# Kernel tuning notes

Hardware: AMD Instinct MI355X
Metric: run time of the kernel (lower is better)

The kernel has to match this reference:

```python
import jax, jax.numpy as jnp
import numpy as np
import math

B, S, D = 4, 2048, 1024

def setup_inputs() -> dict:
    key = jax.random.key(0)
    ks = jax.random.split(key, 8)
    scale = 1.0 / math.sqrt(D)
    x = jax.random.normal(ks[0], (B, S, D), dtype=jnp.float32)
    # additive causal mask: 0 on/below diag, -1e9 above (broadcast over batch)
    causal = jnp.where(jnp.tril(jnp.ones((S, S), dtype=bool)), 0.0, -1e9).astype(jnp.float32)
    mask = jnp.broadcast_to(causal, (B, S, S))
    Wq = jax.random.uniform(ks[1], (D, D), jnp.float32, -scale, scale)
    bq = jax.random.uniform(ks[2], (D,), jnp.float32, -scale, scale)
    Wk = jax.random.uniform(ks[3], (D, D), jnp.float32, -scale, scale)
    bk = jax.random.uniform(ks[4], (D,), jnp.float32, -scale, scale)
    Wv = jax.random.uniform(ks[5], (D, D), jnp.float32, -scale, scale)
    bv = jax.random.uniform(ks[6], (D,), jnp.float32, -scale, scale)
    return {"x": x, "mask": mask, "Wq": Wq, "bq": bq, "Wk": Wk, "bk": bk, "Wv": Wv, "bv": bv}

def reference(x, mask, Wq, bq, Wk, bk, Wv, bv):
    q = jnp.einsum('bsd,de->bse', x, Wq) + bq
    k = jnp.einsum('bsd,de->bse', x, Wk) + bk
    v = jnp.einsum('bsd,de->bse', x, Wv) + bv
    scores = jnp.einsum('bqd,bkd->bqk', q, k) / math.sqrt(k.shape[-1])
    attn = jax.nn.softmax(scores + mask, axis=-1)
    return jnp.einsum('bqk,bkd->bqd', attn, v)
```

## Files before the change

kernel.cpp:

```cpp
#include <hip/hip_runtime.h>
#include <hip/hip_bf16.h>
#include <hip/hip_fp16.h>
#include <math.h>

typedef short v8s __attribute__((ext_vector_type(8)));
typedef short v4s __attribute__((ext_vector_type(4)));
typedef float v4f __attribute__((ext_vector_type(4)));
typedef unsigned short ushort_t;

__device__ __forceinline__ unsigned short f2bf(float f) {
    unsigned int u = __float_as_uint(f);
    u = (u + 0x7FFFu + ((u >> 16) & 1u)) >> 16;
    return (unsigned short)u;
}
__device__ __forceinline__ unsigned short f2h(float f) {
    __half h = __float2half(f);
    return *reinterpret_cast<unsigned short*>(&h);
}
__device__ __forceinline__ float h2f(unsigned short u) {
    __half h = *reinterpret_cast<__half*>(&u);
    return __half2float(h);
}

__device__ __forceinline__ void load_lds16(const void* g, void* l) {
    __builtin_amdgcn_global_load_lds((const __attribute__((address_space(1))) void*)g,
                                     (__attribute__((address_space(3))) void*)l,
                                     16, 0, 0);
}

#define FENCE() asm volatile("" ::: "memory")
#define BAR() do { FENCE(); __builtin_amdgcn_s_barrier(); FENCE(); } while (0)
#define LGKM0() asm volatile("s_waitcnt lgkmcnt(0)" ::: "memory")
#define VMC(n) asm volatile("s_waitcnt vmcnt(" #n ")" ::: "memory")

__global__ __launch_bounds__(256)
void prep_kernel(const float4* __restrict__ x4, ushort_t* __restrict__ xb,
                 const float* __restrict__ W0, const float* __restrict__ W1,
                 const float* __restrict__ W2, ushort_t* __restrict__ Wt) {
    if (blockIdx.x < 2048) {
        int i = blockIdx.x * 256 + threadIdx.x;
        #pragma unroll
        for (int it = 0; it < 4; ++it, i += 524288) {
            float4 v = x4[i];
            v4s p;
            p[0] = (short)f2bf(v.x); p[1] = (short)f2bf(v.y);
            p[2] = (short)f2bf(v.z); p[3] = (short)f2bf(v.w);
            *(v4s*)(xb + (size_t)i * 4) = p;
        }
    } else {
        int f = blockIdx.x - 2048;
        int z = f >> 10; int rem = f & 1023;
        int n0 = (rem & 31) * 32, k0 = (rem >> 5) * 32;
        const float* W = (z == 0) ? W0 : (z == 1 ? W1 : W2);
        ushort_t* out = Wt + (size_t)z * 1024 * 1024;
        __shared__ float tile[32][33];
        int tx = threadIdx.x & 31, ty = threadIdx.x >> 5;
        #pragma unroll
        for (int i2 = 0; i2 < 32; i2 += 8)
            tile[ty + i2][tx] = W[(size_t)(k0 + ty + i2) * 1024 + n0 + tx];
        __syncthreads();
        #pragma unroll
        for (int i2 = 0; i2 < 32; i2 += 8)
            out[(size_t)(n0 + ty + i2) * 1024 + k0 + tx] = f2bf(tile[tx][ty + i2]);
    }
}

__global__ __launch_bounds__(512)
void gemm8_qkv(const ushort_t* __restrict__ A, const ushort_t* __restrict__ Bt,
               const float* __restrict__ bq, const float* __restrict__ bk,
               const float* __restrict__ bv,
               ushort_t* __restrict__ Qb, ushort_t* __restrict__ Kb,
               ushort_t* __restrict__ Vt)
{
    int f = blockIdx.x;
    int xcd = f & 7, i = f >> 3;
    const int by = xcd * 4 + (i >> 4);
    const int bx = i & 15;

    const int tid = threadIdx.x;
    const int lane = tid & 63, wid = tid >> 6;
    const int wm = wid >> 2, wc = wid & 3;
    const int frow = lane & 15, fq4 = lane >> 4;
    const bool bstager = (wid < 6);

    const int brow = by * 256, bcol = bx * 192;

    __shared__ ushort_t LA[2][2][256 * 32];
    __shared__ ushort_t LB[2][2][192 * 32];

    v4f acc[8][3];
    #pragma unroll
    for (int mi = 0; mi < 8; ++mi)
        #pragma unroll
        for (int ni = 0; ni < 3; ++ni)
            acc[mi][ni] = (v4f)0.f;

    const int srr = tid >> 2, sch = tid & 3;
    auto STA = [&](ushort_t* dst, int t, int kh) {
        #pragma unroll
        for (int c = 0; c < 2; ++c) {
            int r = c * 128 + srr;
            int ch = sch ^ ((r >> 1) & 3);
            load_lds16(A + (size_t)(brow + r) * 1024 + t * 64 + kh * 32 + ch * 8,
                       dst + (size_t)(c * 128 + srr) * 32 + sch * 8);
        }
    };
    auto STB = [&](ushort_t* dst, int t, int kh) {
        if (bstager) {
            #pragma unroll
            for (int c = 0; c < 2; ++c) {
                int ck = c * 384 + tid;
                int r = ck >> 2, s = ck & 3;
                int ch = s ^ ((r >> 1) & 3);
                load_lds16(Bt + (size_t)(bcol + r) * 1024 + t * 64 + kh * 32 + ch * 8,
                           dst + (size_t)ck * 8);
            }
        }
    };

    v8s a[4], b[3];
    const int rsw = fq4 ^ ((frow >> 1) & 3);
    auto RDA = [&](int buf, int kh, int mh) {
        #pragma unroll
        for (int i2 = 0; i2 < 4; ++i2) {
            int r = wm * 128 + (mh * 4 + i2) * 16 + frow;
            a[i2] = *(const v8s*)(&LA[buf][kh][(size_t)r * 32 + rsw * 8]);
        }
    };
    auto RDB = [&](int buf, int kh) {
        #pragma unroll
        for (int i2 = 0; i2 < 3; ++i2) {
            int r = wc * 48 + i2 * 16 + frow;
            b[i2] = *(const v8s*)(&LB[buf][kh][(size_t)r * 32 + rsw * 8]);
        }
    };
    auto MM = [&](int mh) {
        __builtin_amdgcn_s_setprio(1);
        #pragma unroll
        for (int i2 = 0; i2 < 4; ++i2)
            #pragma unroll
            for (int n = 0; n < 3; ++n)
                acc[mh * 4 + i2][n] =
                    __builtin_amdgcn_mfma_f32_16x16x32_bf16(a[i2], b[n], acc[mh * 4 + i2][n], 0, 0, 0);
        __builtin_amdgcn_s_setprio(0);
    };
    auto WAIT2 = [&]() { if (bstager) { VMC(4); } else { VMC(2); } };

    STA(LA[0][0], 0, 0); STB(LB[0][0], 0, 0);
    STA(LA[0][1], 0, 1); STB(LB[0][1], 0, 1);
    STA(LA[1][0], 1, 0); STB(LB[1][0], 1, 0);
    WAIT2(); BAR();

    for (int u = 0; u < 8; ++u) {
        const int t0 = 2 * u, t1 = 2 * u + 1;
        const bool pf = (u < 7);
        RDA(0, 0, 0); RDB(0, 0); STA(LA[1][1], t1, 1);
        BAR(); LGKM0(); MM(0); BAR();
        RDA(0, 0, 1); STB(LB[1][1], t1, 1);
        BAR(); LGKM0(); MM(1); BAR();
        RDA(0, 1, 0); RDB(0, 1); if (pf) STA(LA[0][0], t0 + 2, 0);
        BAR(); LGKM0(); MM(0); BAR();
        RDA(0, 1, 1);
        if (pf) { STB(LB[0][0], t0 + 2, 0); WAIT2(); }
        else    { VMC(0); }
        BAR(); LGKM0(); MM(1); BAR();
        RDA(1, 0, 0); RDB(1, 0); if (pf) STA(LA[0][1], t0 + 2, 1);
        BAR(); LGKM0(); MM(0); BAR();
        RDA(1, 0, 1); if (pf) STB(LB[0][1], t0 + 2, 1);
        BAR(); LGKM0(); MM(1); BAR();
        RDA(1, 1, 0); RDB(1, 1); if (pf) STA(LA[1][0], t1 + 2, 0);
        BAR(); LGKM0(); MM(0); BAR();
        RDA(1, 1, 1); if (pf) { STB(LB[1][0], t1 + 2, 0); WAIT2(); }
        BAR(); LGKM0(); MM(1); BAR();
    }

    const int fr = lane & 15;
    const int fq = lane >> 4;
    #pragma unroll
    for (int ni = 0; ni < 3; ++ni) {
        int gc = bx * 192 + wc * 48 + ni * 16 + fr;
        int route = gc >> 10;
        int cg = gc & 1023;
        if (route < 2) {
            ushort_t* C = route ? Kb : Qb;
            float bb = (route ? bk : bq)[cg];
            float scale = route ? 1.0f : 0.03125f;
            #pragma unroll
            for (int mi = 0; mi < 8; ++mi) {
                int gr0 = brow + wm * 128 + mi * 16 + fq * 4;
                #pragma unroll
                for (int j = 0; j < 4; ++j)
                    C[(size_t)(gr0 + j) * 1024 + cg] = f2bf((acc[mi][ni][j] + bb) * scale);
            }
        } else {
            float bb = bv[cg];
            #pragma unroll
            for (int mi = 0; mi < 8; ++mi) {
                int gr0 = brow + wm * 128 + mi * 16 + fq * 4;
                int bbat = gr0 >> 11;
                int sl2 = gr0 & 2047;
                alignas(8) ushort_t tmp[4];
                #pragma unroll
                for (int j = 0; j < 4; ++j)
                    tmp[j] = f2bf(acc[mi][ni][j] + bb);
                *(v4s*)(Vt + (size_t)bbat * (1024 * 2048) + (size_t)cg * 2048 + sl2) =
                    *(const v4s*)tmp;
            }
        }
    }
}

template <int MODE>
__global__ __launch_bounds__(256)
void gemm_ring(const ushort_t* __restrict__ A, int lda, long long strideA,
               const ushort_t* __restrict__ Bt, int ldb, long long strideB,
               void* __restrict__ Cv, int ldc, long long strideC, int K)
{
    int bx, by, bz;
    int f = blockIdx.x;
    if constexpr (MODE == 2) {
        int swz = (f & 7) * 68 + (f >> 3);
        bz = swz / 136; int t = swz % 136;
        int r = (int)((sqrtf(8.f * (float)t + 1.f) - 1.f) * 0.5f);
        while ((r + 1) * (r + 2) / 2 <= t) ++r;
        while (r * (r + 1) / 2 > t) --r;
        by = r; bx = t - r * (r + 1) / 2;
    } else {
        int swz = (f & 7) * 64 + (f >> 3);
        bz = swz >> 7; int rem = swz & 127;
        by = 15 - (rem >> 3); bx = rem & 7;
    }

    const int tid = threadIdx.x;
    const int lane = tid & 63, wid = tid >> 6;
    const int wm = wid >> 1, wc = wid & 1;

    const ushort_t* Ab = A + (size_t)bz * strideA;
    const ushort_t* Bb = Bt + (size_t)bz * strideB;

    __shared__ ushort_t As[3][128 * 32];
    __shared__ ushort_t Bs[3][128 * 32];

    const int brow = by * 128, bcol = bx * 128;

    int kEnd = K;
    if constexpr (MODE == 3) { int lim = (by + 1) * 128; kEnd = lim < K ? lim : K; }
    const int nt = kEnd / 32;

    v4f acc[4][4];
    #pragma unroll
    for (int mi = 0; mi < 4; ++mi)
        #pragma unroll
        for (int ni = 0; ni < 4; ++ni)
            acc[mi][ni] = (v4f)0.f;

    const int rr = tid >> 2, slot = tid & 3;
    auto STAGE = [&](int buf, int t) {
        const int k0 = t * 32;
        #pragma unroll
        for (int c = 0; c < 2; ++c) {
            int r = c * 64 + rr;
            int sc = ((slot ^ ((r >> 1) & 3)) << 3);
            load_lds16(Ab + (size_t)(brow + r) * lda + k0 + sc,
                       &As[buf][(size_t)(c * 64 + wid * 16) * 32]);
        }
        #pragma unroll
        for (int c = 0; c < 2; ++c) {
            int r = c * 64 + rr;
            int sc = ((slot ^ ((r >> 1) & 3)) << 3);
            load_lds16(Bb + (size_t)(bcol + r) * ldb + k0 + sc,
                       &Bs[buf][(size_t)(c * 64 + wid * 16) * 32]);
        }
    };

    const int frow = lane & 15, fq4 = lane >> 4;
    const int csw = ((fq4 ^ ((frow >> 1) & 3)) << 3);

    STAGE(0, 0);
    if (nt > 1) STAGE(1, 1);

    int cur = 0;
    for (int t = 0; t < nt; ++t) {
        if (t + 1 < nt) VMC(4); else VMC(0);
        BAR();
        if (t + 2 < nt) {
            int tgt = cur ? cur - 1 : 2;
            STAGE(tgt, t + 2);
        }
        const ushort_t* Ac = &As[cur][0];
        const ushort_t* Bc = &Bs[cur][0];
        v8s a[4], b[4];
        #pragma unroll
        for (int mi = 0; mi < 4; ++mi)
            a[mi] = *(const v8s*)(Ac + (size_t)(wm * 64 + mi * 16 + frow) * 32 + csw);
        #pragma unroll
        for (int ni = 0; ni < 4; ++ni)
            b[ni] = *(const v8s*)(Bc + (size_t)(wc * 64 + ni * 16 + frow) * 32 + csw);
        __builtin_amdgcn_s_setprio(1);
        #pragma unroll
        for (int mi = 0; mi < 4; ++mi)
            #pragma unroll
            for (int ni = 0; ni < 4; ++ni)
                acc[mi][ni] = __builtin_amdgcn_mfma_f32_16x16x32_bf16(a[mi], b[ni], acc[mi][ni], 0, 0, 0);
        __builtin_amdgcn_s_setprio(0);
        cur = (cur == 2) ? 0 : cur + 1;
    }

    const int fr = lane & 15;
    const int fq = lane >> 4;
    if constexpr (MODE == 2) {
        ushort_t* C = (ushort_t*)Cv + (size_t)bz * strideC;
        #pragma unroll
        for (int ni = 0; ni < 4; ++ni) {
            int gc = bcol + wc * 64 + ni * 16 + fr;
            #pragma unroll
            for (int mi = 0; mi < 4; ++mi) {
                int gr0 = brow + wm * 64 + mi * 16 + fq * 4;
                #pragma unroll
                for (int j = 0; j < 4; ++j)
                    C[(size_t)(gr0 + j) * ldc + gc] = f2h(acc[mi][ni][j]);
            }
        }
    } else {
        float* C = (float*)Cv + (size_t)bz * strideC;
        #pragma unroll
        for (int ni = 0; ni < 4; ++ni) {
            int gc = bcol + wc * 64 + ni * 16 + fr;
            #pragma unroll
            for (int mi = 0; mi < 4; ++mi) {
                int gr0 = brow + wm * 64 + mi * 16 + fq * 4;
                #pragma unroll
                for (int j = 0; j < 4; ++j)
                    C[(size_t)(gr0 + j) * ldc + gc] = acc[mi][ni][j];
            }
        }
    }
}

__global__ __launch_bounds__(256) void softmax_causal(ushort_t* __restrict__ Sc) {
    const int wid = threadIdx.x >> 6, lane = threadIdx.x & 63;
    const int row = blockIdx.x * 4 + wid;
    const int b = row >> 11, i = row & 2047;
    ushort_t* srow = Sc + ((size_t)b * 2048 + i) * 2048;
    const int L = i + 1;
    const int Lw = ((i >> 7) + 1) << 7;
    const int C4 = Lw >> 2;

    float v[8][4];
    const int NS = (C4 + 63) >> 6;

    float mx = -3.0e38f;
    #pragma unroll 8
    for (int s = 0; s < NS; ++s) {
        int c = lane + s * 64;
        if (c < C4) {
            v4s u = *(const v4s*)(srow + c * 4);
            #pragma unroll
            for (int e = 0; e < 4; ++e) {
                int j = c * 4 + e;
                float t = (j < L) ? h2f((unsigned short)u[e]) : -3.0e38f;
                v[s][e] = t;
                mx = fmaxf(mx, t);
            }
        }
    }
    #pragma unroll
    for (int o = 32; o; o >>= 1) mx = fmaxf(mx, __shfl_xor(mx, o));

    float sum = 0.f;
    #pragma unroll 8
    for (int s = 0; s < NS; ++s) {
        int c = lane + s * 64;
        if (c < C4) {
            #pragma unroll
            for (int e = 0; e < 4; ++e) {
                int j = c * 4 + e;
                float ev = (j < L) ? __expf(v[s][e] - mx) : 0.f;
                v[s][e] = ev;
                sum += ev;
            }
        }
    }
    #pragma unroll
    for (int o = 32; o; o >>= 1) sum += __shfl_xor(sum, o);
    const float inv = 1.f / sum;

    #pragma unroll 8
    for (int s = 0; s < NS; ++s) {
        int c = lane + s * 64;
        if (c < C4) {
            v4s p;
            #pragma unroll
            for (int e = 0; e < 4; ++e)
                p[e] = (short)f2bf(v[s][e] * inv);
            *(v4s*)(srow + c * 4) = p;
        }
    }
}

extern "C" void kernel_launch(void* const* d_in, const int* in_sizes, int n_in,
                              void* d_out, int out_size, void* d_ws, size_t ws_size,
                              hipStream_t stream) {
    const float* x  = (const float*)d_in[0];
    const float* Wq = (const float*)d_in[2];
    const float* bq = (const float*)d_in[3];
    const float* Wk = (const float*)d_in[4];
    const float* bk = (const float*)d_in[5];
    const float* Wv = (const float*)d_in[6];
    const float* bv = (const float*)d_in[7];

    ushort_t* xb = (ushort_t*)d_ws;
    ushort_t* Wt = xb + (size_t)8192 * 1024;
    ushort_t* Qb = Wt + (size_t)3 * 1024 * 1024;
    ushort_t* Kb = Qb + (size_t)8192 * 1024;
    ushort_t* Vt = Kb + (size_t)8192 * 1024;
    ushort_t* Sc = Vt + (size_t)8192 * 1024;

    prep_kernel<<<5120, 256, 0, stream>>>((const float4*)x, xb, Wq, Wk, Wv, Wt);

    gemm8_qkv<<<512, 512, 0, stream>>>(xb, Wt, bq, bk, bv, Qb, Kb, Vt);

    gemm_ring<2><<<544, 256, 0, stream>>>(Qb, 1024, 2048LL * 1024,
                                          Kb, 1024, 2048LL * 1024,
                                          Sc, 2048, 2048LL * 2048, 1024);

    softmax_causal<<<2048, 256, 0, stream>>>(Sc);

    gemm_ring<3><<<512, 256, 0, stream>>>(Sc, 2048, 2048LL * 2048,
                                          Vt, 2048, 2048LL * 1024,
                                          d_out, 1024, 2048LL * 1024, 2048);
    (void)in_sizes; (void)n_in; (void)out_size; (void)ws_size;
}
```

Baseline: 160.9 us.

## Switch QKV GEMM to 32x32x16 MFMA with 128x384 block tiles

The fused QKV projection GEMM now issues 32x32x16 bf16 MFMAs instead of 16x16x32, and the block tile changes from 256x192 to 128x384. LDS staging, fragment reads, the swizzle and the epilogue indexing are reworked to fit the new layout, and all 8 waves now stage B. Larger MFMAs cut the instruction count and the LDS fragment reads per flop. The new tile shape changes reuse and how many blocks the grid has, which may affect load balance.

```diff
diff --git a/kernel.cpp b/kernel.cpp
--- a/kernel.cpp
+++ b/kernel.cpp
@@ -6,6 +6,7 @@
 typedef short v8s __attribute__((ext_vector_type(8)));
 typedef short v4s __attribute__((ext_vector_type(4)));
 typedef float v4f __attribute__((ext_vector_type(4)));
+typedef float v16f __attribute__((ext_vector_type(16)));
 typedef unsigned short ushort_t;
 
 __device__ __forceinline__ unsigned short f2bf(float f) {
@@ -74,82 +75,81 @@
 {
     int f = blockIdx.x;
     int xcd = f & 7, i = f >> 3;
-    const int by = xcd * 4 + (i >> 4);
-    const int bx = i & 15;
+    const int by = xcd * 8 + (i >> 3);
+    const int bx = i & 7;
 
     const int tid = threadIdx.x;
     const int lane = tid & 63, wid = tid >> 6;
     const int wm = wid >> 2, wc = wid & 3;
-    const int frow = lane & 15, fq4 = lane >> 4;
-    const bool bstager = (wid < 6);
-
-    const int brow = by * 256, bcol = bx * 192;
-
-    __shared__ ushort_t LA[2][2][256 * 32];
-    __shared__ ushort_t LB[2][2][192 * 32];
-
-    v4f acc[8][3];
+    const int l31 = lane & 31, l5 = lane >> 5;
+
+    const int brow = by * 128, bcol = bx * 384;
+
+    __shared__ ushort_t LA[2][2][128 * 32];
+    __shared__ ushort_t LB[2][2][384 * 32];
+
+    v16f acc[2][3];
     #pragma unroll
-    for (int mi = 0; mi < 8; ++mi)
+    for (int mh = 0; mh < 2; ++mh)
         #pragma unroll
         for (int ni = 0; ni < 3; ++ni)
-            acc[mi][ni] = (v4f)0.f;
+            acc[mh][ni] = (v16f)0.f;
 
     const int srr = tid >> 2, sch = tid & 3;
     auto STA = [&](ushort_t* dst, int t, int kh) {
-        #pragma unroll
-        for (int c = 0; c < 2; ++c) {
-            int r = c * 128 + srr;
-            int ch = sch ^ ((r >> 1) & 3);
-            load_lds16(A + (size_t)(brow + r) * 1024 + t * 64 + kh * 32 + ch * 8,
-                       dst + (size_t)(c * 128 + srr) * 32 + sch * 8);
-        }
+        int r = srr;
+        int ch = sch ^ ((r >> 1) & 3);
+        load_lds16(A + (size_t)(brow + r) * 1024 + t * 64 + kh * 32 + ch * 8,
+                   dst + (size_t)r * 32 + sch * 8);
     };
     auto STB = [&](ushort_t* dst, int t, int kh) {
-        if (bstager) {
-            #pragma unroll
-            for (int c = 0; c < 2; ++c) {
-                int ck = c * 384 + tid;
-                int r = ck >> 2, s = ck & 3;
-                int ch = s ^ ((r >> 1) & 3);
-                load_lds16(Bt + (size_t)(bcol + r) * 1024 + t * 64 + kh * 32 + ch * 8,
-                           dst + (size_t)ck * 8);
-            }
-        }
-    };
-
-    v8s a[4], b[3];
-    const int rsw = fq4 ^ ((frow >> 1) & 3);
+        #pragma unroll
+        for (int c = 0; c < 3; ++c) {
+            int ck = c * 512 + tid;
+            int r = ck >> 2, s = ck & 3;
+            int ch = s ^ ((r >> 1) & 3);
+            load_lds16(Bt + (size_t)(bcol + r) * 1024 + t * 64 + kh * 32 + ch * 8,
+                       dst + (size_t)ck * 8);
+        }
+    };
+
+    v8s a[2], b[3][2];
     auto RDA = [&](int buf, int kh, int mh) {
-        #pragma unroll
-        for (int i2 = 0; i2 < 4; ++i2) {
-            int r = wm * 128 + (mh * 4 + i2) * 16 + frow;
-            a[i2] = *(const v8s*)(&LA[buf][kh][(size_t)r * 32 + rsw * 8]);
+        int r = wm * 64 + mh * 32 + l31;
+        int sw = (r >> 1) & 3;
+        #pragma unroll
+        for (int ks = 0; ks < 2; ++ks) {
+            int c = (ks * 2 + l5) ^ sw;
+            a[ks] = *(const v8s*)(&LA[buf][kh][(size_t)r * 32 + c * 8]);
         }
     };
     auto RDB = [&](int buf, int kh) {
         #pragma unroll
-        for (int i2 = 0; i2 < 3; ++i2) {
-            int r = wc * 48 + i2 * 16 + frow;
-            b[i2] = *(const v8s*)(&LB[buf][kh][(size_t)r * 32 + rsw * 8]);
+        for (int ni = 0; ni < 3; ++ni) {
+            int r = wc * 96 + ni * 32 + l31;
+            int sw = (r >> 1) & 3;
+            #pragma unroll
+            for (int ks = 0; ks < 2; ++ks) {
+                int c = (ks * 2 + l5) ^ sw;
+                b[ni][ks] = *(const v8s*)(&LB[buf][kh][(size_t)r * 32 + c * 8]);
+            }
         }
     };
     auto MM = [&](int mh) {
         __builtin_amdgcn_s_setprio(1);
         #pragma unroll
-        for (int i2 = 0; i2 < 4; ++i2)
-            #pragma unroll
-            for (int n = 0; n < 3; ++n)
-                acc[mh * 4 + i2][n] =
-                    __builtin_amdgcn_mfma_f32_16x16x32_bf16(a[i2], b[n], acc[mh * 4 + i2][n], 0, 0, 0);
+        for (int ni = 0; ni < 3; ++ni)
+            #pragma unroll
+            for (int ks = 0; ks < 2; ++ks)
+                acc[mh][ni] = __builtin_amdgcn_mfma_f32_32x32x16_bf16(
+                    a[ks], b[ni][ks], acc[mh][ni], 0, 0, 0);
         __builtin_amdgcn_s_setprio(0);
     };
-    auto WAIT2 = [&]() { if (bstager) { VMC(4); } else { VMC(2); } };
 
     STA(LA[0][0], 0, 0); STB(LB[0][0], 0, 0);
     STA(LA[0][1], 0, 1); STB(LB[0][1], 0, 1);
     STA(LA[1][0], 1, 0); STB(LB[1][0], 1, 0);
-    WAIT2(); BAR();
+    VMC(4); BAR();
 
     for (int u = 0; u < 8; ++u) {
         const int t0 = 2 * u, t1 = 2 * u + 1;
@@ -161,7 +161,7 @@
         RDA(0, 1, 0); RDB(0, 1); if (pf) STA(LA[0][0], t0 + 2, 0);
         BAR(); LGKM0(); MM(0); BAR();
         RDA(0, 1, 1);
-        if (pf) { STB(LB[0][0], t0 + 2, 0); WAIT2(); }
+        if (pf) { STB(LB[0][0], t0 + 2, 0); VMC(4); }
         else    { VMC(0); }
         BAR(); LGKM0(); MM(1); BAR();
         RDA(1, 0, 0); RDB(1, 0); if (pf) STA(LA[0][1], t0 + 2, 1);
@@ -170,41 +170,44 @@
         BAR(); LGKM0(); MM(1); BAR();
         RDA(1, 1, 0); RDB(1, 1); if (pf) STA(LA[1][0], t1 + 2, 0);
         BAR(); LGKM0(); MM(0); BAR();
-        RDA(1, 1, 1); if (pf) { STB(LB[1][0], t1 + 2, 0); WAIT2(); }
+        RDA(1, 1, 1); if (pf) { STB(LB[1][0], t1 + 2, 0); VMC(4); }
         BAR(); LGKM0(); MM(1); BAR();
     }
 
-    const int fr = lane & 15;
-    const int fq = lane >> 4;
     #pragma unroll
-    for (int ni = 0; ni < 3; ++ni) {
-        int gc = bx * 192 + wc * 48 + ni * 16 + fr;
-        int route = gc >> 10;
-        int cg = gc & 1023;
-        if (route < 2) {
-            ushort_t* C = route ? Kb : Qb;
-            float bb = (route ? bk : bq)[cg];
-            float scale = route ? 1.0f : 0.03125f;
-            #pragma unroll
-            for (int mi = 0; mi < 8; ++mi) {
-                int gr0 = brow + wm * 128 + mi * 16 + fq * 4;
+    for (int mh = 0; mh < 2; ++mh) {
+        #pragma unroll
+        for (int ni = 0; ni < 3; ++ni) {
+            int gc = bcol + wc * 96 + ni * 32 + l31;
+            int route = gc >> 10;
+            int cg = gc & 1023;
+            int grb = brow + wm * 64 + mh * 32 + 4 * l5;
+            if (route < 2) {
+                ushort_t* C = route ? Kb : Qb;
+                float bb = (route ? bk : bq)[cg];
+                float scale = route ? 1.0f : 0.03125f;
                 #pragma unroll
-                for (int j = 0; j < 4; ++j)
-                    C[(size_t)(gr0 + j) * 1024 + cg] = f2bf((acc[mi][ni][j] + bb) * scale);
-            }
-        } else {
-            float bb = bv[cg];
-            #pragma unroll
-            for (int mi = 0; mi < 8; ++mi) {
-                int gr0 = brow + wm * 128 + mi * 16 + fq * 4;
-                int bbat = gr0 >> 11;
-                int sl2 = gr0 & 2047;
-                alignas(8) ushort_t tmp[4];
+                for (int q = 0; q < 4; ++q) {
+                    #pragma unroll
+                    for (int jj = 0; jj < 4; ++jj) {
+                        int gr = grb + 8 * q + jj;
+                        C[(size_t)gr * 1024 + cg] =
+                            f2bf((acc[mh][ni][q * 4 + jj] + bb) * scale);
+                    }
+                }
+            } else {
+                float bb = bv[cg];
+                int bbat = grb >> 11;
                 #pragma unroll
-                for (int j = 0; j < 4; ++j)
-                    tmp[j] = f2bf(acc[mi][ni][j] + bb);
-                *(v4s*)(Vt + (size_t)bbat * (1024 * 2048) + (size_t)cg * 2048 + sl2) =
-                    *(const v4s*)tmp;
+                for (int q = 0; q < 4; ++q) {
+                    int s0 = (grb + 8 * q) & 2047;
+                    alignas(8) ushort_t tmp[4];
+                    #pragma unroll
+                    for (int jj = 0; jj < 4; ++jj)
+                        tmp[jj] = f2bf(acc[mh][ni][q * 4 + jj] + bb);
+                    *(v4s*)(Vt + (size_t)bbat * (1024 * 2048) +
+                            (size_t)cg * 2048 + s0) = *(const v4s*)tmp;
+                }
             }
         }
     }
```

Result: slower. 178.1 us (+10.7%).
